# Optimization experiments

Hardware: AMD Instinct MI355X
Metric: run time of the kernel (lower is better)

The kernel has to match this reference:

```python
import jax, jax.numpy as jnp
import numpy as np

NEG_INF = -1.0e9  # matches torch masked_fill value


def setup_inputs() -> dict:
    key = jax.random.key(0)
    kq, kk, kv, km = jax.random.split(key, 4)
    B, S, D = 16, 2048, 256
    q = jax.random.normal(kq, (B, S, D), dtype=jnp.float32)
    k = jax.random.normal(kk, (B, D, S), dtype=jnp.float32)  # pre-transposed keys
    v = jax.random.normal(kv, (B, S, D), dtype=jnp.float32)
    mask = jax.random.randint(km, (B, 1, S), 0, 2, dtype=jnp.int32)
    return {"q": q, "k": k, "v": v, "mask": mask}


def reference(q, k, v, mask):
    # q: [B, n_q, d], k: [B, d, n_k], v: [B, n_k, n_dv]
    n_dk = k.shape[1]
    att = jnp.matmul(q, k)                      # [B, n_q, n_k]
    att = jnp.where(mask == 0, NEG_INF, att)    # masked_fill(mask==0, -1e9)
    # NOTE: faithful to source — scale applied AFTER softmax
    att = jax.nn.softmax(att, axis=-1) / jnp.asarray(n_dk, att.dtype) ** 0.5
    out = jnp.matmul(att, v)                    # [B, n_q, n_dv]
    return jnp.transpose(out, (0, 2, 1))        # [B, n_dv, n_q]
```

## Files before the change

kernel.cpp:

```cpp
#include <hip/hip_runtime.h>

typedef _Float16 half8 __attribute__((ext_vector_type(8)));
typedef float floatx16 __attribute__((ext_vector_type(16)));

#define B_  16
#define S_  2048
#define D_  256
#define LOG2E 1.4426950408889634f

__device__ __forceinline__ void dma16(const _Float16* g, _Float16* l) {
    __builtin_amdgcn_global_load_lds(
        (const __attribute__((address_space(1))) void*)g,
        (__attribute__((address_space(3))) void*)l, 16, 0, 0);
}

__device__ __forceinline__ void tr_body(const float* __restrict__ ib,
                                        _Float16* __restrict__ ob,
                                        int Rin, int Cin, int swz,
                                        int c0, int r0, _Float16* tl, int t)
{
    const int rr = t >> 4, cc = (t & 15) * 4;
    #pragma unroll
    for (int p = 0; p < 4; ++p) {
        const float4 x = *(const float4*)(ib + (size_t)(r0 + rr + 16*p) * Cin + c0 + cc);
        tl[(cc+0)*72 + rr + 16*p] = (_Float16)x.x;
        tl[(cc+1)*72 + rr + 16*p] = (_Float16)x.y;
        tl[(cc+2)*72 + rr + 16*p] = (_Float16)x.z;
        tl[(cc+3)*72 + rr + 16*p] = (_Float16)x.w;
    }
    __syncthreads();
    #pragma unroll
    for (int u = 0; u < 2; ++u) {
        const int idx  = t + 256*u;
        const int jloc = idx >> 3, lc = idx & 7;
        const half8 h = *(const half8*)(tl + jloc*72 + 8*lc);
        const int jg  = c0 + jloc;
        const int lco = swz ? (lc ^ ((jg >> 1) & 7)) : lc;
        *(half8*)(ob + (size_t)jg * Rin + r0 + 8*lco) = h;
    }
}

__global__ __launch_bounds__(256)
void tr_both(const float* __restrict__ k, const float* __restrict__ v,
             _Float16* __restrict__ kt, _Float16* __restrict__ vtp)
{
    __shared__ _Float16 tl[64 * 72];
    const int id   = blockIdx.x;
    const int isV  = id >> 11;
    const int rem  = id & 2047;
    const int z    = rem >> 7;
    const int t128 = rem & 127;
    if (!isV) {
        const int c0 = (t128 & 31) * 64, r0 = (t128 >> 5) * 64;
        tr_body(k + (size_t)z * D_ * S_, kt + (size_t)z * S_ * D_,
                D_, S_, 1, c0, r0, tl, threadIdx.x);
    } else {
        const int c0 = (t128 & 3) * 64, r0 = (t128 >> 2) * 64;
        tr_body(v + (size_t)z * S_ * D_, vtp + (size_t)z * S_ * D_,
                S_, D_, 0, c0, r0, tl, threadIdx.x);
    }
}

__global__ __launch_bounds__(512, 2)
void attn_v10(const float* __restrict__ q, const _Float16* __restrict__ kts,
              const _Float16* __restrict__ vt, const int* __restrict__ mask,
              float* __restrict__ out)
{
    __shared__ _Float16 kb[2][2][32 * D_];
    __shared__ _Float16 vb[2][2][D_ * 32];
    __shared__ float    mneg[2048];
    __shared__ float    statM[4*32], statL[4*32];

    const int tid   = threadIdx.x;
    const int w     = tid >> 6;
    const int strip = w & 3;
    const int half  = w >> 2;
    const int lane  = tid & 63;
    const int jl    = lane & 31;
    const int h     = lane >> 5;
    const int pj    = (jl >> 1) & 7;

    const int bx   = blockIdx.x;
    const int rest = bx >> 3;
    const int b    = 2 * (bx & 7) + (rest >> 4);
    const int qg   = rest & 15;
    const int i0   = qg * 128 + 32 * strip;

    const float*    qb  = q    + (size_t)b * S_ * D_;
    const _Float16* ktb = kts  + (size_t)b * S_ * D_;
    const _Float16* vtb = vt   + (size_t)b * S_ * D_;
    const int*      mb  = mask + (size_t)b * S_;
    float*          ob  = out  + (size_t)b * D_ * S_;

    #pragma unroll
    for (int u = 0; u < 4; ++u) {
        const int i  = tid + 512*u;
        const int tg = i >> 5, hh = (i >> 4) & 1, r = i & 15;
        const int kv = 32*tg + (r&3) + 8*(r>>2) + 4*hh;
        mneg[i] = mb[kv] ? 0.0f : -1.0e9f;
    }

    half8 qf[16];
    {
        const float* qrow = qb + (size_t)(i0 + jl) * D_;
        #pragma unroll
        for (int s = 0; s < 16; ++s) {
            const float4 a = *(const float4*)(qrow + 16*s + 8*h);
            const float4 c = *(const float4*)(qrow + 16*s + 8*h + 4);
            half8 v;
            v[0]=(_Float16)a.x; v[1]=(_Float16)a.y; v[2]=(_Float16)a.z; v[3]=(_Float16)a.w;
            v[4]=(_Float16)c.x; v[5]=(_Float16)c.y; v[6]=(_Float16)c.z; v[7]=(_Float16)c.w;
            qf[s] = v;
        }
    }

    floatx16 o[8];
    #pragma unroll
    for (int nt = 0; nt < 8; ++nt) o[nt] = (floatx16){};
    float M = -3.0e38f, lsum = 0.0f;

    const int vrow = lane >> 2;
    const int vco  = 8 * ((lane & 3) ^ (vrow & 3));
    const int vo0 = jl*32 + (((0 + h) ^ (jl & 3)) * 8);
    const int vo1 = jl*32 + (((2 + h) ^ (jl & 3)) * 8);

    const int j0base = half * 1024;

    auto stage = [&](int tile, int buf) {
        const int j0 = j0base + tile * 32;
        _Float16* kd = kb[half][buf];
        #pragma unroll
        for (int m = 0; m < 4; ++m)
            dma16(ktb + (size_t)(j0 + 8*strip + 2*m) * D_ + lane*8,
                  kd + (8*strip + 2*m) * D_);
        _Float16* vd = vb[half][buf];
        #pragma unroll
        for (int m = 0; m < 4; ++m)
            dma16(vtb + (size_t)(64*strip + 16*m + vrow) * S_ + j0 + vco,
                  vd + (64*strip + 16*m) * 32);
    };

    auto pkf = [](float a, float bf) -> int {
        auto t = __builtin_amdgcn_cvt_pkrtz(a, bf);
        return __builtin_bit_cast(int, t);
    };
    auto xsw = [&](int a, int bf, int& lo, int& hi) {
        const int ax = __shfl_xor(a, 32, 64);
        const int bx = __shfl_xor(bf, 32, 64);
        lo = h ? bx : a;
        hi = h ? bf : ax;
    };

    stage(0, 0);
    asm volatile("s_waitcnt vmcnt(0) lgkmcnt(0)\n\ts_barrier" ::: "memory");

    for (int tt = 0; tt < 32; ++tt) {
        if (tt < 31) stage(tt + 1, (tt + 1) & 1);

        const _Float16* kc = kb[half][tt & 1];
        const _Float16* vc = vb[half][tt & 1];
        const int tg = half*32 + tt;

        floatx16 sa = (floatx16){}, sb = (floatx16){};
        __builtin_amdgcn_s_setprio(1);
        #pragma unroll
        for (int s = 0; s < 16; s += 2) {
            const half8 k0 = *(const half8*)(kc + jl*D_ + 8*((2*s     + h) ^ pj));
            const half8 k1 = *(const half8*)(kc + jl*D_ + 8*((2*s + 2 + h) ^ pj));
            sa = __builtin_amdgcn_mfma_f32_32x32x16_f16(k0, qf[s],   sa, 0,0,0);
            sb = __builtin_amdgcn_mfma_f32_32x32x16_f16(k1, qf[s+1], sb, 0,0,0);
        }
        __builtin_amdgcn_s_setprio(0);

        const float4* mrow = (const float4*)(mneg + (tg*2 + h)*16);
        const float4 m0 = mrow[0], m1 = mrow[1], m2 = mrow[2], m3 = mrow[3];
        float sv[16];
        sv[0]=sa[0]+sb[0]+m0.x;  sv[1]=sa[1]+sb[1]+m0.y;
        sv[2]=sa[2]+sb[2]+m0.z;  sv[3]=sa[3]+sb[3]+m0.w;
        sv[4]=sa[4]+sb[4]+m1.x;  sv[5]=sa[5]+sb[5]+m1.y;
        sv[6]=sa[6]+sb[6]+m1.z;  sv[7]=sa[7]+sb[7]+m1.w;
        sv[8]=sa[8]+sb[8]+m2.x;  sv[9]=sa[9]+sb[9]+m2.y;
        sv[10]=sa[10]+sb[10]+m2.z; sv[11]=sa[11]+sb[11]+m2.w;
        sv[12]=sa[12]+sb[12]+m3.x; sv[13]=sa[13]+sb[13]+m3.y;
        sv[14]=sa[14]+sb[14]+m3.z; sv[15]=sa[15]+sb[15]+m3.w;

        float c0 = fmaxf(fmaxf(fmaxf(sv[0],sv[1]),fmaxf(sv[2],sv[3])),
                         fmaxf(fmaxf(sv[4],sv[5]),fmaxf(sv[6],sv[7])));
        float c1 = fmaxf(fmaxf(fmaxf(sv[8],sv[9]),fmaxf(sv[10],sv[11])),
                         fmaxf(fmaxf(sv[12],sv[13]),fmaxf(sv[14],sv[15])));
        float cm = fmaxf(c0, c1);
        cm = fmaxf(cm, __shfl_xor(cm, 32, 64));
        if (__any(cm > M + 8.0f)) {
            const float Mn = fmaxf(M, cm);
            const float al = __builtin_amdgcn_exp2f((M - Mn) * LOG2E);
            M = Mn; lsum *= al;
            #pragma unroll
            for (int nt = 0; nt < 8; ++nt)
                #pragma unroll
                for (int r = 0; r < 16; ++r) o[nt][r] *= al;
        }

        float p[16];
        #pragma unroll
        for (int r = 0; r < 16; ++r)
            p[r] = __builtin_amdgcn_exp2f((sv[r] - M) * LOG2E);
        lsum += (((p[0]+p[1])+(p[2]+p[3]))+((p[4]+p[5])+(p[6]+p[7])))
              + (((p[8]+p[9])+(p[10]+p[11]))+((p[12]+p[13])+(p[14]+p[15])));

        union H8 { int i[4]; half8 h8; } pa0u, pa1u;
        xsw(pkf(p[0],p[1]),   pkf(p[4],p[5]),   pa0u.i[0], pa0u.i[2]);
        xsw(pkf(p[2],p[3]),   pkf(p[6],p[7]),   pa0u.i[1], pa0u.i[3]);
        xsw(pkf(p[8],p[9]),   pkf(p[12],p[13]), pa1u.i[0], pa1u.i[2]);
        xsw(pkf(p[10],p[11]), pkf(p[14],p[15]), pa1u.i[1], pa1u.i[3]);

        __builtin_amdgcn_s_setprio(1);
        #pragma unroll
        for (int nt = 0; nt < 8; ++nt) {
            const half8 vf0 = *(const half8*)(vc + nt*1024 + vo0);
            const half8 vf1 = *(const half8*)(vc + nt*1024 + vo1);
            o[nt] = __builtin_amdgcn_mfma_f32_32x32x16_f16(vf0, pa0u.h8, o[nt], 0,0,0);
            o[nt] = __builtin_amdgcn_mfma_f32_32x32x16_f16(vf1, pa1u.h8, o[nt], 0,0,0);
        }
        __builtin_amdgcn_s_setprio(0);

        asm volatile("s_waitcnt vmcnt(0) lgkmcnt(0)\n\ts_barrier" ::: "memory");
    }

    const float lT = lsum + __shfl_xor(lsum, 32, 64);
    float* ms = (strip < 2) ? ((float*)kb + strip * 8192)
                            : ((float*)vb + (strip - 2) * 8192);
    if (half == 1) {
        #pragma unroll
        for (int nt = 0; nt < 8; ++nt)
            #pragma unroll
            for (int r = 0; r < 16; ++r)
                ms[(nt*16 + r)*64 + lane] = o[nt][r];
        if (h == 0) { statM[strip*32 + jl] = M; statL[strip*32 + jl] = lT; }
    }
    __syncthreads();
    if (half == 0) {
        const float MB = statM[strip*32 + jl];
        const float lB = statL[strip*32 + jl];
        const float Mm = fmaxf(M, MB);
        const float aA = __builtin_amdgcn_exp2f((M  - Mm) * LOG2E);
        const float aB = __builtin_amdgcn_exp2f((MB - Mm) * LOG2E);
        const float osc = 1.0f / (16.0f * (aA*lT + aB*lB));
        #pragma unroll
        for (int nt = 0; nt < 8; ++nt) {
            #pragma unroll
            for (int r = 0; r < 16; ++r) {
                const int d = 32*nt + (r&3) + 8*(r>>2) + 4*h;
                ob[(size_t)d * S_ + i0 + jl] =
                    (aA*o[nt][r] + aB*ms[(nt*16 + r)*64 + lane]) * osc;
            }
        }
    }
}

extern "C" void kernel_launch(void* const* d_in, const int* in_sizes, int n_in,
                              void* d_out, int out_size, void* d_ws, size_t ws_size,
                              hipStream_t stream)
{
    const float* q    = (const float*)d_in[0];
    const float* k    = (const float*)d_in[1];
    const float* v    = (const float*)d_in[2];
    const int*   mask = (const int*)d_in[3];
    float*       out  = (float*)d_out;

    _Float16* kt  = (_Float16*)d_ws;
    _Float16* vtp = kt + (size_t)B_ * S_ * D_;

    tr_both<<<dim3(4096), dim3(256), 0, stream>>>(k, v, kt, vtp);
    attn_v10<<<dim3(B_ * (S_/128)), dim3(512), 0, stream>>>(q, kt, vtp, mask, out);
}
```

Baseline: 280.7 us.

## Software-pipeline PV MFMA one tile behind QK and retune LDS swizzles

Restructures the attention loop so each iteration computes QK for the current tile and then the PV product for the previous tile. This lets the softmax of one tile overlap with matrix work and gives the V loads an extra stage to arrive. K and V staging are split so V for the next tile is issued only after its buffer has been consumed, behind a partial vmcnt wait, and a PV epilogue handles the final tile. The K and V LDS XOR swizzles change (K by row&7, V by (row>>1)&3) to cut bank conflicts. The QK accumulation now uses a single MFMA dependency chain, which may lengthen latency, and the extra barrier per iteration adds sync cost.

```diff
diff --git a/kernel.cpp b/kernel.cpp
--- a/kernel.cpp
+++ b/kernel.cpp
@@ -35,7 +35,7 @@
         const int jloc = idx >> 3, lc = idx & 7;
         const half8 h = *(const half8*)(tl + jloc*72 + 8*lc);
         const int jg  = c0 + jloc;
-        const int lco = swz ? (lc ^ ((jg >> 1) & 7)) : lc;
+        const int lco = swz ? (lc ^ (jg & 7)) : lc;
         *(half8*)(ob + (size_t)jg * Rin + r0 + 8*lco) = h;
     }
 }
@@ -62,7 +62,7 @@
 }
 
 __global__ __launch_bounds__(512, 2)
-void attn_v10(const float* __restrict__ q, const _Float16* __restrict__ kts,
+void attn_v11(const float* __restrict__ q, const _Float16* __restrict__ kts,
               const _Float16* __restrict__ vt, const int* __restrict__ mask,
               float* __restrict__ out)
 {
@@ -78,7 +78,7 @@
     const int lane  = tid & 63;
     const int jl    = lane & 31;
     const int h     = lane >> 5;
-    const int pj    = (jl >> 1) & 7;
+    const int pj    = jl & 7;
 
     const int bx   = blockIdx.x;
     const int rest = bx >> 3;
@@ -120,19 +120,22 @@
     float M = -3.0e38f, lsum = 0.0f;
 
     const int vrow = lane >> 2;
-    const int vco  = 8 * ((lane & 3) ^ (vrow & 3));
-    const int vo0 = jl*32 + (((0 + h) ^ (jl & 3)) * 8);
-    const int vo1 = jl*32 + (((2 + h) ^ (jl & 3)) * 8);
+    const int vco  = 8 * ((lane & 3) ^ ((lane >> 3) & 3));
+    const int vo0 = jl*32 + 8*((0 + h) ^ ((jl >> 1) & 3));
+    const int vo1 = jl*32 + 8*((2 + h) ^ ((jl >> 1) & 3));
 
     const int j0base = half * 1024;
 
-    auto stage = [&](int tile, int buf) {
+    auto stageK = [&](int tile, int buf) {
         const int j0 = j0base + tile * 32;
         _Float16* kd = kb[half][buf];
         #pragma unroll
         for (int m = 0; m < 4; ++m)
             dma16(ktb + (size_t)(j0 + 8*strip + 2*m) * D_ + lane*8,
                   kd + (8*strip + 2*m) * D_);
+    };
+    auto stageV = [&](int tile, int buf) {
+        const int j0 = j0base + tile * 32;
         _Float16* vd = vb[half][buf];
         #pragma unroll
         for (int m = 0; m < 4; ++m)
@@ -151,38 +154,47 @@
         hi = h ? bf : ax;
     };
 
-    stage(0, 0);
+    union H8 { int i[4]; half8 h8; };
+    H8 paA0, paA1, paB0, paB1;
+
+    stageK(0, 0);
+    stageV(0, 0);
     asm volatile("s_waitcnt vmcnt(0) lgkmcnt(0)\n\ts_barrier" ::: "memory");
 
     for (int tt = 0; tt < 32; ++tt) {
-        if (tt < 31) stage(tt + 1, (tt + 1) & 1);
+        if (tt < 31) stageK(tt + 1, (tt + 1) & 1);
 
         const _Float16* kc = kb[half][tt & 1];
-        const _Float16* vc = vb[half][tt & 1];
+        floatx16 sc = (floatx16){};
+        __builtin_amdgcn_s_setprio(1);
+        #pragma unroll
+        for (int s = 0; s < 16; ++s) {
+            const half8 k0 = *(const half8*)(kc + jl*D_ + 8*((2*s + h) ^ pj));
+            sc = __builtin_amdgcn_mfma_f32_32x32x16_f16(k0, qf[s], sc, 0,0,0);
+        }
+        __builtin_amdgcn_s_setprio(0);
+
+        if (tt > 0) {
+            const _Float16* vc = vb[half][(tt - 1) & 1];
+            __builtin_amdgcn_s_setprio(1);
+            #pragma unroll
+            for (int nt = 0; nt < 8; ++nt) {
+                const half8 vf0 = *(const half8*)(vc + nt*1024 + vo0);
+                const half8 vf1 = *(const half8*)(vc + nt*1024 + vo1);
+                o[nt] = __builtin_amdgcn_mfma_f32_32x32x16_f16(vf0, paA0.h8, o[nt], 0,0,0);
+                o[nt] = __builtin_amdgcn_mfma_f32_32x32x16_f16(vf1, paA1.h8, o[nt], 0,0,0);
+            }
+            __builtin_amdgcn_s_setprio(0);
+        }
+
         const int tg = half*32 + tt;
-
-        floatx16 sa = (floatx16){}, sb = (floatx16){};
-        __builtin_amdgcn_s_setprio(1);
-        #pragma unroll
-        for (int s = 0; s < 16; s += 2) {
-            const half8 k0 = *(const half8*)(kc + jl*D_ + 8*((2*s     + h) ^ pj));
-            const half8 k1 = *(const half8*)(kc + jl*D_ + 8*((2*s + 2 + h) ^ pj));
-            sa = __builtin_amdgcn_mfma_f32_32x32x16_f16(k0, qf[s],   sa, 0,0,0);
-            sb = __builtin_amdgcn_mfma_f32_32x32x16_f16(k1, qf[s+1], sb, 0,0,0);
-        }
-        __builtin_amdgcn_s_setprio(0);
-
         const float4* mrow = (const float4*)(mneg + (tg*2 + h)*16);
         const float4 m0 = mrow[0], m1 = mrow[1], m2 = mrow[2], m3 = mrow[3];
         float sv[16];
-        sv[0]=sa[0]+sb[0]+m0.x;  sv[1]=sa[1]+sb[1]+m0.y;
-        sv[2]=sa[2]+sb[2]+m0.z;  sv[3]=sa[3]+sb[3]+m0.w;
-        sv[4]=sa[4]+sb[4]+m1.x;  sv[5]=sa[5]+sb[5]+m1.y;
-        sv[6]=sa[6]+sb[6]+m1.z;  sv[7]=sa[7]+sb[7]+m1.w;
-        sv[8]=sa[8]+sb[8]+m2.x;  sv[9]=sa[9]+sb[9]+m2.y;
-        sv[10]=sa[10]+sb[10]+m2.z; sv[11]=sa[11]+sb[11]+m2.w;
-        sv[12]=sa[12]+sb[12]+m3.x; sv[13]=sa[13]+sb[13]+m3.y;
-        sv[14]=sa[14]+sb[14]+m3.z; sv[15]=sa[15]+sb[15]+m3.w;
+        sv[0]=sc[0]+m0.x;  sv[1]=sc[1]+m0.y;  sv[2]=sc[2]+m0.z;  sv[3]=sc[3]+m0.w;
+        sv[4]=sc[4]+m1.x;  sv[5]=sc[5]+m1.y;  sv[6]=sc[6]+m1.z;  sv[7]=sc[7]+m1.w;
+        sv[8]=sc[8]+m2.x;  sv[9]=sc[9]+m2.y;  sv[10]=sc[10]+m2.z; sv[11]=sc[11]+m2.w;
+        sv[12]=sc[12]+m3.x; sv[13]=sc[13]+m3.y; sv[14]=sc[14]+m3.z; sv[15]=sc[15]+m3.w;
 
         float c0 = fmaxf(fmaxf(fmaxf(sv[0],sv[1]),fmaxf(sv[2],sv[3])),
                          fmaxf(fmaxf(sv[4],sv[5]),fmaxf(sv[6],sv[7])));
@@ -207,24 +219,30 @@
         lsum += (((p[0]+p[1])+(p[2]+p[3]))+((p[4]+p[5])+(p[6]+p[7])))
               + (((p[8]+p[9])+(p[10]+p[11]))+((p[12]+p[13])+(p[14]+p[15])));
 
-        union H8 { int i[4]; half8 h8; } pa0u, pa1u;
-        xsw(pkf(p[0],p[1]),   pkf(p[4],p[5]),   pa0u.i[0], pa0u.i[2]);
-        xsw(pkf(p[2],p[3]),   pkf(p[6],p[7]),   pa0u.i[1], pa0u.i[3]);
-        xsw(pkf(p[8],p[9]),   pkf(p[12],p[13]), pa1u.i[0], pa1u.i[2]);
-        xsw(pkf(p[10],p[11]), pkf(p[14],p[15]), pa1u.i[1], pa1u.i[3]);
-
-        __builtin_amdgcn_s_setprio(1);
+        xsw(pkf(p[0],p[1]),   pkf(p[4],p[5]),   paB0.i[0], paB0.i[2]);
+        xsw(pkf(p[2],p[3]),   pkf(p[6],p[7]),   paB0.i[1], paB0.i[3]);
+        xsw(pkf(p[8],p[9]),   pkf(p[12],p[13]), paB1.i[0], paB1.i[2]);
+        xsw(pkf(p[10],p[11]), pkf(p[14],p[15]), paB1.i[1], paB1.i[3]);
+        paA0 = paB0; paA1 = paB1;
+
+        asm volatile("s_waitcnt lgkmcnt(0)\n\ts_barrier" ::: "memory");
+        if (tt < 31) stageV(tt + 1, (tt + 1) & 1);
+        asm volatile("s_waitcnt vmcnt(4) lgkmcnt(0)\n\ts_barrier" ::: "memory");
+    }
+
+    asm volatile("s_waitcnt vmcnt(0)" ::: "memory");
+    __syncthreads();
+    {
+        const _Float16* vc = vb[half][1];
         #pragma unroll
         for (int nt = 0; nt < 8; ++nt) {
             const half8 vf0 = *(const half8*)(vc + nt*1024 + vo0);
             const half8 vf1 = *(const half8*)(vc + nt*1024 + vo1);
-            o[nt] = __builtin_amdgcn_mfma_f32_32x32x16_f16(vf0, pa0u.h8, o[nt], 0,0,0);
-            o[nt] = __builtin_amdgcn_mfma_f32_32x32x16_f16(vf1, pa1u.h8, o[nt], 0,0,0);
-        }
-        __builtin_amdgcn_s_setprio(0);
-
-        asm volatile("s_waitcnt vmcnt(0) lgkmcnt(0)\n\ts_barrier" ::: "memory");
-    }
+            o[nt] = __builtin_amdgcn_mfma_f32_32x32x16_f16(vf0, paA0.h8, o[nt], 0,0,0);
+            o[nt] = __builtin_amdgcn_mfma_f32_32x32x16_f16(vf1, paA1.h8, o[nt], 0,0,0);
+        }
+    }
+    __syncthreads();
 
     const float lT = lsum + __shfl_xor(lsum, 32, 64);
     float* ms = (strip < 2) ? ((float*)kb + strip * 8192)
@@ -271,5 +289,5 @@
     _Float16* vtp = kt + (size_t)B_ * S_ * D_;
 
     tr_both<<<dim3(4096), dim3(256), 0, stream>>>(k, v, kt, vtp);
-    attn_v10<<<dim3(B_ * (S_/128)), dim3(512), 0, stream>>>(q, kt, vtp, mask, out);
-}
+    attn_v11<<<dim3(B_ * (S_/128)), dim3(512), 0, stream>>>(q, kt, vtp, mask, out);
+}
```

Result: faster. 266.6 us (-5.0%).
